# Kernel tuning notes

Measured on AMD Instinct MI355X. Metric: run time of the kernel, lower is better.

The kernel has to match this reference:

```python
import math
import jax, jax.numpy as jnp
import numpy as np

EPS_LN = 1e-5
EPS_NORM = 1e-12


def conv2d(x, w, b=None, groups=1):
    # x: (B,C,H,W), w: (O, I//groups, kh, kw)
    out = jax.lax.conv_general_dilated(
        x, w, window_strides=(1, 1), padding='SAME',
        dimension_numbers=('NCHW', 'OIHW', 'NCHW'),
        feature_group_count=groups)
    if b is not None:
        out = out + b[None, :, None, None]
    return out


def layernorm2d(x, w, b):
    # LayerNorm over channel dim of (B,C,H,W)
    mu = x.mean(axis=1, keepdims=True)
    var = ((x - mu) ** 2).mean(axis=1, keepdims=True)
    xn = (x - mu) / jnp.sqrt(var + EPS_LN)
    return xn * w[None, :, None, None] + b[None, :, None, None]


def l2norm(x):
    n = jnp.sqrt((x * x).sum(axis=-1, keepdims=True))
    return x / jnp.maximum(n, EPS_NORM)


def mha(s, Wi, bi, Wo, bo, num_heads):
    # torch nn.MultiheadAttention (batch_first) self-attention
    B, S, C = s.shape
    Dh = C // num_heads
    qkv = s @ Wi.T + bi                      # (B,S,3C)
    q, k, v = jnp.split(qkv, 3, axis=-1)
    hd = lambda t: t.reshape(B, S, num_heads, Dh).transpose(0, 2, 1, 3)
    q, k, v = hd(q), hd(k), hd(v)            # (B,H,S,Dh)
    attn = jax.nn.softmax(jnp.einsum('bhqd,bhkd->bhqk', q, k) / math.sqrt(Dh), axis=-1)
    o = jnp.einsum('bhqk,bhkd->bhqd', attn, v).transpose(0, 2, 1, 3).reshape(B, S, C)
    return o @ Wo.T + bo


def frfn(x, pconv_w, lin1_w, lin1_b, dw_w, dw_b, lin2_w, lin2_b):
    b, c, h, w = x.shape
    dc = c // 4
    x1 = conv2d(x[:, :dc], pconv_w)                       # partial conv, no bias
    x = jnp.concatenate([x1, x[:, dc:]], axis=1)
    xt = x.transpose(0, 2, 3, 1).reshape(b, h * w, c)
    y = jax.nn.gelu(xt @ lin1_w.T + lin1_b, approximate=False)  # (b,hw,2*hid)
    y1, y2 = jnp.split(y, 2, axis=-1)
    hid = lin1_w.shape[0] // 2
    y1 = y1.reshape(b, h, w, hid).transpose(0, 3, 1, 2)
    y1 = jax.nn.gelu(conv2d(y1, dw_w, dw_b, groups=hid), approximate=False)
    y1 = y1.transpose(0, 2, 3, 1).reshape(b, h * w, hid)
    out = (y1 * y2) @ lin2_w.T + lin2_b
    return out.reshape(b, h, w, c).transpose(0, 3, 1, 2)


def setup_inputs() -> dict:
    key = jax.random.key(0)
    ks = jax.random.split(key, 10)
    B, C, H, W = 16, 256, 64, 64
    HID = 2 * C  # FRFN hidden = embed_dim*2
    DC = C // 4
    w = lambda k, shape: (jax.random.normal(k, shape, dtype=jnp.float32) * 0.02)
    return {
        'x': jax.random.normal(ks[0], (B, C, H, W), dtype=jnp.float32),
        'slot_scale': jnp.asarray(C ** -0.5, dtype=jnp.float32),
        'norm1_w': jnp.ones((C,), jnp.float32), 'norm1_b': jnp.zeros((C,), jnp.float32),
        'in_proj_w': w(ks[1], (3 * C, C)), 'in_proj_b': jnp.zeros((3 * C,), jnp.float32),
        'out_proj_w': w(ks[2], (C, C)), 'out_proj_b': jnp.zeros((C,), jnp.float32),
        'norm2_w': jnp.ones((C,), jnp.float32), 'norm2_b': jnp.zeros((C,), jnp.float32),
        'pconv_w': w(ks[3], (DC, DC, 3, 3)),
        'lin1_w': w(ks[4], (2 * HID, C)), 'lin1_b': jnp.zeros((2 * HID,), jnp.float32),
        'dw_w': w(ks[5], (HID, 1, 3, 3)), 'dw_b': jnp.zeros((HID,), jnp.float32),
        'lin2_w': w(ks[6], (C, HID)), 'lin2_b': jnp.zeros((C,), jnp.float32),
    }


def reference(x, slot_scale, norm1_w, norm1_b, in_proj_w, in_proj_b,
              out_proj_w, out_proj_b, norm2_w, norm2_b,
              pconv_w, lin1_w, lin1_b, dw_w, dw_b, lin2_w, lin2_b):
    NUM_HEADS, POOL = 8, 8
    b, c, h, w = x.shape
    copy = x
    # ada_avgpool slot init: 8x8 exact block means (h,w divisible by pool)
    pooled = x.reshape(b, c, POOL, h // POOL, POOL, w // POOL).mean(axis=(3, 5))  # (b,c,8,8)
    init_slots = pooled.transpose(0, 2, 3, 1).reshape(b, POOL * POOL, c)          # (b,S,c)

    shortcut = x
    xn = layernorm2d(x, norm1_w, norm1_b)
    xf = xn.transpose(0, 2, 3, 1).reshape(b, h * w, c)                            # (b,N,c)
    logits = slot_scale * jnp.einsum('bsc,bnc->bsn', l2norm(init_slots), l2norm(xf))
    slots = jnp.einsum('bsn,bnc->bsc', jax.nn.softmax(logits, axis=-1), xf)
    slots = mha(slots, in_proj_w, in_proj_b, out_proj_w, out_proj_b, NUM_HEADS)
    out = jnp.einsum('bns,bsc->bnc', jax.nn.softmax(logits.transpose(0, 2, 1), axis=-1), slots)
    out = out.transpose(0, 2, 1).reshape(b, c, h, w)

    x = shortcut + out
    x = x + frfn(layernorm2d(x, norm2_w, norm2_b),
                 pconv_w, lin1_w, lin1_b, dw_w, dw_b, lin2_w, lin2_b)
    return (x, copy - x)
```

## Files before the change

### kernel.cpp

```cpp
#include <hip/hip_runtime.h>
#include <hip/hip_bf16.h>
#include <stdint.h>
#include <math.h>

#define BB 16
#define CC 256
#define HH 64
#define WW 64
#define NN 4096
#define SS 64
#define NHEAD 8
#define DH 32
#define HID 512
#define DC 64

typedef float    f32x4  __attribute__((ext_vector_type(4)));
typedef float    f32x2  __attribute__((ext_vector_type(2)));
typedef uint32_t u32x4  __attribute__((ext_vector_type(4)));
typedef uint16_t u16x8  __attribute__((ext_vector_type(8)));
typedef uint16_t u16x4  __attribute__((ext_vector_type(4)));
typedef uint16_t u16x2  __attribute__((ext_vector_type(2)));

__device__ __forceinline__ float gelu_fast(float x){
  float z = x * (1.5957691216057308f + 0.07135481627613705f * x * x);
  float e = __expf(z);
  float r = __builtin_amdgcn_rcpf(e + 1.0f);
  return x * e * r;
}
__device__ __forceinline__ uint16_t f2b(float f){
  union { float f; uint32_t u; } v; v.f = f;
  uint32_t r = v.u + 0x7fffu + ((v.u >> 16) & 1u);
  return (uint16_t)(r >> 16);
}
__device__ __forceinline__ float b2f(uint16_t h){
  union { uint32_t u; float f; } v; v.u = ((uint32_t)h) << 16;
  return v.f;
}
__device__ __forceinline__ f32x2 bpair(uint32_t u){
  union { uint32_t u; float f; } lo, hi;
  lo.u = u << 16; hi.u = u & 0xffff0000u;
  return (f32x2){lo.f, hi.f};
}

__device__ __forceinline__ float waveSum(float v){
#pragma unroll
  for (int m = 32; m >= 1; m >>= 1) v += __shfl_xor(v, m, 64);
  return v;
}
__device__ __forceinline__ float blockSum256(float v, float* s4){
  v = waveSum(v);
  __syncthreads();
  if ((threadIdx.x & 63) == 0) s4[threadIdx.x >> 6] = v;
  __syncthreads();
  return s4[0] + s4[1] + s4[2] + s4[3];
}

__device__ __forceinline__ void g2l16(const void* g, void* l){
  __builtin_amdgcn_global_load_lds((const __attribute__((address_space(1))) uint32_t*)g,
                                   (__attribute__((address_space(3))) uint32_t*)l, 16, 0, 0);
}

__device__ __forceinline__ int swz8(int row, int kp){ return (kp ^ (row & 7)) << 3; }

__device__ __forceinline__ void mfma_bf16(f32x4& d, u16x8 a, u16x8 b){
  asm volatile("v_mfma_f32_16x16x32_bf16 %0, %1, %2, %0" : "+v"(d) : "v"(a), "v"(b));
}

template<int SWA, int SWB>
__device__ __forceinline__ void mma_core(const uint16_t* lA, int lda, const uint16_t* lB, int ldb,
                                         f32x4 (&acc)[4][4], int wrow, int wcol, int lane){
  const int rb = lane & 15, ub = lane >> 4;
#pragma unroll
  for (int ks = 0; ks < 2; ks++){
    const int u = ks * 4 + ub;
    u16x8 af[4], bf[4];
#pragma unroll
    for (int m = 0; m < 4; m++){
      int r = wrow + m * 16 + rb;
      int e = SWA ? ((u ^ (r & 7)) << 3) : (u << 3);
      af[m] = *(const u16x8*)&lA[r * lda + e];
    }
#pragma unroll
    for (int n = 0; n < 4; n++){
      int r = wcol + n * 16 + rb;
      int e = SWB ? ((u ^ (r & 7)) << 3) : (u << 3);
      bf[n] = *(const u16x8*)&lB[r * ldb + e];
    }
#pragma unroll
    for (int m = 0; m < 4; m++)
#pragma unroll
      for (int n = 0; n < 4; n++)
        mfma_bf16(acc[m][n], af[m], bf[n]);
  }
}

__global__ __launch_bounds__(256) void k_t2b(const float* __restrict__ in, uint16_t* __restrict__ out){
  __shared__ float tile[64][33];
  int b = blockIdx.z;
  int n0 = blockIdx.x * 32;
  int c0 = blockIdx.y * 64;
  int tx = threadIdx.x, ty = threadIdx.y;
  const float* src = in + (size_t)b * CC * NN;
#pragma unroll
  for (int i = 0; i < 64; i += 8)
    tile[ty + i][tx] = src[(size_t)(c0 + ty + i) * NN + n0 + tx];
  __syncthreads();
  uint16_t* dst = out + (size_t)b * NN * CC;
#pragma unroll
  for (int i = 0; i < 32; i += 8){
    int r = ty + i;
    u16x2 o; o[0] = f2b(tile[tx * 2][r]); o[1] = f2b(tile[tx * 2 + 1][r]);
    *(u16x2*)&dst[(size_t)(n0 + r) * CC + c0 + tx * 2] = o;
  }
}

__global__ __launch_bounds__(256) void k_pool(const uint16_t* __restrict__ xhwcb, uint16_t* __restrict__ slotsNb){
  int bs = blockIdx.x; int b = bs >> 6, s = bs & 63;
  int sy = (s >> 3) * 8, sx = (s & 7) * 8;
  int t = threadIdx.x;
  int c4 = t & 63, pg = t >> 6;
  const uint16_t* base = xhwcb + (size_t)b * NN * CC;
  float a0 = 0.f, a1 = 0.f, a2 = 0.f, a3 = 0.f;
#pragma unroll
  for (int i = 0; i < 16; i++){
    int p = pg * 16 + i; int py = p >> 3, px = p & 7;
    u16x4 v = *(const u16x4*)&base[(size_t)((sy + py) * WW + sx + px) * CC + c4 * 4];
    a0 += b2f(v[0]); a1 += b2f(v[1]); a2 += b2f(v[2]); a3 += b2f(v[3]);
  }
  __shared__ float sm[4][64][4];
  sm[pg][c4][0] = a0; sm[pg][c4][1] = a1; sm[pg][c4][2] = a2; sm[pg][c4][3] = a3;
  __syncthreads();
  if (t < 64){
    float v0 = (sm[0][t][0] + sm[1][t][0] + sm[2][t][0] + sm[3][t][0]) * (1.0f / 64.0f);
    float v1 = (sm[0][t][1] + sm[1][t][1] + sm[2][t][1] + sm[3][t][1]) * (1.0f / 64.0f);
    float v2 = (sm[0][t][2] + sm[1][t][2] + sm[2][t][2] + sm[3][t][2]) * (1.0f / 64.0f);
    float v3 = (sm[0][t][3] + sm[1][t][3] + sm[2][t][3] + sm[3][t][3]) * (1.0f / 64.0f);
    float ss = waveSum(v0 * v0 + v1 * v1 + v2 * v2 + v3 * v3);
    float inv = 1.0f / fmaxf(sqrtf(ss), 1e-12f);
    u16x4 o; o[0] = f2b(v0 * inv); o[1] = f2b(v1 * inv); o[2] = f2b(v2 * inv); o[3] = f2b(v3 * inv);
    *(u16x4*)&slotsNb[(size_t)bs * CC + t * 4] = o;
  }
}

__global__ __launch_bounds__(256) void k_ln_w(const uint16_t* __restrict__ xa, const uint16_t* __restrict__ xb,
                                              const float* __restrict__ w, const float* __restrict__ b,
                                              uint16_t* __restrict__ xoutb, float* __restrict__ rn,
                                              uint16_t* __restrict__ xn2p){
  int row = blockIdx.x * 4 + (threadIdx.x >> 6);
  int lane = threadIdx.x & 63;
  u16x4 va = *(const u16x4*)&xa[(size_t)row * CC + lane * 4];
  float v0 = b2f(va[0]), v1 = b2f(va[1]), v2 = b2f(va[2]), v3 = b2f(va[3]);
  if (xb){
    u16x4 vb = *(const u16x4*)&xb[(size_t)row * CC + lane * 4];
    v0 += b2f(vb[0]); v1 += b2f(vb[1]); v2 += b2f(vb[2]); v3 += b2f(vb[3]);
  }
  float mu = waveSum(v0 + v1 + v2 + v3) * (1.0f / CC);
  float d0 = v0 - mu, d1 = v1 - mu, d2 = v2 - mu, d3 = v3 - mu;
  float var = waveSum(d0 * d0 + d1 * d1 + d2 * d2 + d3 * d3) * (1.0f / CC);
  float inv = rsqrtf(var + 1e-5f);
  float4 wv = *(const float4*)&w[lane * 4];
  float4 bv = *(const float4*)&b[lane * 4];
  float x0 = d0 * inv * wv.x + bv.x;
  float x1 = d1 * inv * wv.y + bv.y;
  float x2 = d2 * inv * wv.z + bv.z;
  float x3 = d3 * inv * wv.w + bv.w;
  u16x4 o; o[0] = f2b(x0); o[1] = f2b(x1); o[2] = f2b(x2); o[3] = f2b(x3);
  *(u16x4*)&xoutb[(size_t)row * CC + lane * 4] = o;
  if (xn2p && lane < 16){
    int bb = row >> 12, n = row & 4095, y = n >> 6, x = n & 63;
    *(u16x4*)&xn2p[(((size_t)(bb * 66 + y + 1)) * 66 + x + 1) * 64 + lane * 4] = o;
  }
  if (rn){
    float ss = waveSum(x0 * x0 + x1 * x1 + x2 * x2 + x3 * x3);
    if (lane == 0) rn[row] = 1.0f / fmaxf(sqrtf(ss), 1e-12f);
  }
}

__global__ __launch_bounds__(256) void k_zb(uint16_t* __restrict__ xn2p){
  int i = blockIdx.x * 256 + threadIdx.x;
  if (i >= 16 * 260 * 16) return;
  int c4 = i & 15; int rest = i >> 4;
  int j = rest % 260; int b = rest / 260;
  int py, px;
  if (j < 66){ py = 0; px = j; }
  else if (j < 132){ py = 65; px = j - 66; }
  else if (j < 196){ py = j - 132 + 1; px = 0; }
  else { py = j - 196 + 1; px = 65; }
  u16x4 z; z[0] = 0; z[1] = 0; z[2] = 0; z[3] = 0;
  *(u16x4*)&xn2p[(((size_t)(b * 66 + py)) * 66 + px) * 64 + c4 * 4] = z;
}

__global__ __launch_bounds__(256) void k_cvtw(const float* __restrict__ wi, const float* __restrict__ wo,
                                              const float* __restrict__ w1, const float* __restrict__ w2,
                                              const float* __restrict__ pw, const float* __restrict__ dww,
                                              uint16_t* __restrict__ wib, uint16_t* __restrict__ wob,
                                              uint16_t* __restrict__ w1b, uint16_t* __restrict__ w2b,
                                              uint16_t* __restrict__ wp2, float* __restrict__ dwwT){
  int i = blockIdx.x * 256 + threadIdx.x;
  if (i < 163840){
    const float* src; uint16_t* dst; int off;
    if (i < 49152){ src = wi; dst = wib; off = i; }
    else if (i < 65536){ src = wo; dst = wob; off = i - 49152; }
    else if (i < 131072){ src = w1; dst = w1b; off = i - 65536; }
    else { src = w2; dst = w2b; off = i - 131072; }
    float4 v = ((const float4*)src)[off];
    u16x4 o;
    o[0] = f2b(v.x); o[1] = f2b(v.y); o[2] = f2b(v.z); o[3] = f2b(v.w);
    *(u16x4*)&dst[(size_t)off * 4] = o;
  } else if (i < 200704){
    int j = i - 163840;
    if (j < 64 * 576){
      int co = j / 576, r = j % 576, tap = r >> 6, ci = r & 63;
      wp2[j] = f2b(pw[(size_t)co * 576 + ci * 9 + tap]);
    }
  } else {
    int j = i - 200704;
    if (j < 9 * HID){
      int tap = j / HID, ch = j % HID;
      dwwT[j] = dww[(size_t)ch * 9 + tap];
    }
  }
}

__global__ __launch_bounds__(256) void k_txT(const uint16_t* __restrict__ xnb, uint16_t* __restrict__ xnTb){
  __shared__ uint16_t tile[64 * 66];
  int b = blockIdx.z;
  int n0 = blockIdx.x * 64, c0 = blockIdx.y * 64;
  int t = threadIdx.x;
#pragma unroll
  for (int i = 0; i < 16; i++){
    int idx = i * 256 + t;
    int nr = idx >> 6, c = idx & 63;
    tile[c * 66 + nr] = xnb[((size_t)b * NN + n0 + nr) * CC + c0 + c];
  }
  __syncthreads();
#pragma unroll
  for (int i = 0; i < 16; i++){
    int idx = i * 256 + t;
    int cr = idx >> 6, n = idx & 63;
    xnTb[((size_t)b * CC + c0 + cr) * NN + n0 + n] = tile[cr * 66 + n];
  }
}

__global__ __launch_bounds__(256) void k_logits_mfma(const uint16_t* __restrict__ slotsNb,
                                                     const uint16_t* __restrict__ xnb,
                                                     const float* __restrict__ rn,
                                                     const float* __restrict__ scale_p,
                                                     uint16_t* __restrict__ E){
  __shared__ uint16_t smem[20480];
  __shared__ float rnS[256];
  uint16_t* lA = smem;
  uint16_t* lB = smem + 64 * 64;
  int t = threadIdx.x, lane = t & 63, w = t >> 6;
  int b = blockIdx.y, n0 = blockIdx.x * 256;
  rnS[t] = rn[b * NN + n0 + t];
  f32x4 acc[4][4];
#pragma unroll
  for (int m = 0; m < 4; m++)
#pragma unroll
    for (int n = 0; n < 4; n++) acc[m][n] = (f32x4){0.f, 0.f, 0.f, 0.f};
  for (int kc = 0; kc < 4; kc++){
#pragma unroll
    for (int i = 0; i < 2; i++){
      int idx = i * 256 + t, row = idx >> 3, kp = idx & 7;
      *(u16x8*)&lA[row * 64 + swz8(row, kp)] = *(const u16x8*)&slotsNb[(size_t)(b * 64 + row) * 256 + kc * 64 + kp * 8];
    }
#pragma unroll
    for (int i = 0; i < 8; i++){
      int idx = i * 256 + t, row = idx >> 3, kp = idx & 7;
      *(u16x8*)&lB[row * 64 + swz8(row, kp)] = *(const u16x8*)&xnb[((size_t)b * NN + n0 + row) * 256 + kc * 64 + kp * 8];
    }
    __syncthreads();
    mma_core<1, 1>(lA, 64, lB, 64, acc, 0, w * 64, lane);
    __syncthreads();
  }
  float scale = scale_p[0];
  int rb4 = (lane >> 4) * 4, cb = lane & 15;
#pragma unroll
  for (int m = 0; m < 4; m++)
#pragma unroll
    for (int n = 0; n < 4; n++)
#pragma unroll
      for (int j = 0; j < 4; j++){
        int s = m * 16 + rb4 + j, nl = w * 64 + n * 16 + cb;
        smem[s * 264 + nl] = f2b(__expf(acc[m][n][j] * scale * rnS[nl]));
      }
  __syncthreads();
#pragma unroll
  for (int i = 0; i < 8; i++){
    int idx = i * 256 + t, row = idx >> 5, cseg = idx & 31;
    *(u16x8*)&E[((size_t)b * 64 + row) * NN + n0 + cseg * 8] = *(const u16x8*)&smem[row * 264 + cseg * 8];
  }
}

__global__ __launch_bounds__(256) void k_z1(const uint16_t* __restrict__ E, float* __restrict__ invz1){
  int bs = blockIdx.x, t = threadIdx.x;
  u16x8 v0 = *(const u16x8*)&E[(size_t)bs * NN + t * 16];
  u16x8 v1 = *(const u16x8*)&E[(size_t)bs * NN + t * 16 + 8];
  float s = 0.f;
#pragma unroll
  for (int i = 0; i < 8; i++) s += b2f(v0[i]) + b2f(v1[i]);
  __shared__ float s4[4];
  float z = blockSum256(s, s4);
  if (t == 0) invz1[bs] = 1.0f / z;
}

__global__ __launch_bounds__(256) void k_slots_mfma(const uint16_t* __restrict__ E,
                                                    const uint16_t* __restrict__ xnTb,
                                                    float* __restrict__ part){
  __shared__ uint16_t lA[64 * 64];
  __shared__ uint16_t lB[256 * 64];
  int t = threadIdx.x, lane = t & 63, w = t >> 6;
  int ks = blockIdx.x, b = blockIdx.y;
  f32x4 acc[4][4];
#pragma unroll
  for (int m = 0; m < 4; m++)
#pragma unroll
    for (int n = 0; n < 4; n++) acc[m][n] = (f32x4){0.f, 0.f, 0.f, 0.f};
  for (int kc = 0; kc < 8; kc++){
    int n0 = ks * 512 + kc * 64;
#pragma unroll
    for (int i = 0; i < 2; i++){
      int q = (w * 2 + i) * 64 + lane;
      int row = q >> 3, kpe = swz8(row, q & 7);
      g2l16(&E[((size_t)b * 64 + row) * NN + n0 + kpe], &lA[(w * 2 + i) * 512]);
    }
#pragma unroll
    for (int i = 0; i < 8; i++){
      int q = (w * 8 + i) * 64 + lane;
      int row = q >> 3, kpe = swz8(row, q & 7);
      g2l16(&xnTb[((size_t)b * CC + row) * NN + n0 + kpe], &lB[(w * 8 + i) * 512]);
    }
    __syncthreads();
    mma_core<1, 1>(lA, 64, lB, 64, acc, 0, w * 64, lane);
    __syncthreads();
  }
  int rb4 = (lane >> 4) * 4, cb = lane & 15;
#pragma unroll
  for (int m = 0; m < 4; m++)
#pragma unroll
    for (int n = 0; n < 4; n++)
#pragma unroll
      for (int j = 0; j < 4; j++){
        int s = m * 16 + rb4 + j, c = w * 64 + n * 16 + cb;
        part[(((size_t)b * 8 + ks) * 64 + s) * 256 + c] = acc[m][n][j];
      }
}

__global__ __launch_bounds__(256) void k_fold(const float* __restrict__ part, const float* __restrict__ invz1,
                                              uint16_t* __restrict__ slotsb){
  int i = blockIdx.x * 256 + threadIdx.x;
  int row = i >> 6, c4 = i & 63;
  int b = row >> 6, s = row & 63;
  float4 a = {0.f, 0.f, 0.f, 0.f};
#pragma unroll
  for (int p = 0; p < 8; p++){
    float4 v = *(const float4*)&part[(((size_t)b * 8 + p) * 64 + s) * 256 + c4 * 4];
    a.x += v.x; a.y += v.y; a.z += v.z; a.w += v.w;
  }
  float iz = invz1[row];
  u16x4 o; o[0] = f2b(a.x * iz); o[1] = f2b(a.y * iz); o[2] = f2b(a.z * iz); o[3] = f2b(a.w * iz);
  *(u16x4*)&slotsb[(size_t)row * 256 + c4 * 4] = o;
}

__global__ __launch_bounds__(256) void k_gemm_qkv(const uint16_t* __restrict__ slotsb,
                                                  const uint16_t* __restrict__ wib,
                                                  const float* __restrict__ bi,
                                                  float* __restrict__ qkv){
  __shared__ uint16_t lA[128 * 64];
  __shared__ uint16_t lB[128 * 64];
  int t = threadIdx.x, lane = t & 63, w = t >> 6;
  int wrow = (w >> 1) * 64, wcol = (w & 1) * 64;
  int BR = blockIdx.x * 128, BC = blockIdx.y * 128;
  f32x4 acc[4][4];
#pragma unroll
  for (int m = 0; m < 4; m++)
#pragma unroll
    for (int n = 0; n < 4; n++) acc[m][n] = (f32x4){0.f, 0.f, 0.f, 0.f};
  for (int kc = 0; kc < 4; kc++){
#pragma unroll
    for (int i = 0; i < 4; i++){
      int idx = i * 256 + t, row = idx >> 3, kp = idx & 7;
      *(u16x8*)&lA[row * 64 + swz8(row, kp)] = *(const u16x8*)&slotsb[(size_t)(BR + row) * 256 + kc * 64 + kp * 8];
      *(u16x8*)&lB[row * 64 + swz8(row, kp)] = *(const u16x8*)&wib[(size_t)(BC + row) * 256 + kc * 64 + kp * 8];
    }
    __syncthreads();
    mma_core<1, 1>(lA, 64, lB, 64, acc, wrow, wcol, lane);
    __syncthreads();
  }
  int rb4 = (lane >> 4) * 4, cb = lane & 15;
#pragma unroll
  for (int m = 0; m < 4; m++)
#pragma unroll
    for (int n = 0; n < 4; n++){
      int c = BC + wcol + n * 16 + cb;
      float bias = bi[c];
#pragma unroll
      for (int j = 0; j < 4; j++)
        qkv[(size_t)(BR + wrow + m * 16 + rb4 + j) * 768 + c] = acc[m][n][j] + bias;
    }
}

__global__ __launch_bounds__(256) void k_attn(const float* __restrict__ qkv, uint16_t* __restrict__ aob){
  int b = blockIdx.x >> 3, h = blockIdx.x & 7;
  __shared__ float lq[64][33], lk[64][33], lv[64][33];
  __shared__ float sc[64][65];
  int t = threadIdx.x;
  for (int idx = t; idx < 64 * 32; idx += 256){
    int s = idx >> 5, d = idx & 31;
    const float* base = qkv + ((size_t)b * SS + s) * 768 + h * DH + d;
    lq[s][d] = base[0];
    lk[s][d] = base[256];
    lv[s][d] = base[512];
  }
  __syncthreads();
  const float rs = 0.17677669529663687f;
  for (int idx = t; idx < 64 * 64; idx += 256){
    int qq = idx >> 6, kk = idx & 63;
    float a = 0.f;
#pragma unroll
    for (int d = 0; d < 32; d++) a += lq[qq][d] * lk[kk][d];
    sc[qq][kk] = a * rs;
  }
  __syncthreads();
  {
    int r = t >> 2, sub = t & 3;
    float m = -1e30f;
#pragma unroll
    for (int k = sub * 16; k < sub * 16 + 16; k++) m = fmaxf(m, sc[r][k]);
    m = fmaxf(m, __shfl_xor(m, 1, 64));
    m = fmaxf(m, __shfl_xor(m, 2, 64));
    float z = 0.f;
#pragma unroll
    for (int k = sub * 16; k < sub * 16 + 16; k++){
      float e = __expf(sc[r][k] - m); sc[r][k] = e; z += e;
    }
    z += __shfl_xor(z, 1, 64);
    z += __shfl_xor(z, 2, 64);
    float iv = 1.0f / z;
#pragma unroll
    for (int k = sub * 16; k < sub * 16 + 16; k++) sc[r][k] *= iv;
  }
  __syncthreads();
  for (int idx = t; idx < 64 * 32; idx += 256){
    int qq = idx >> 5, d = idx & 31;
    float a = 0.f;
#pragma unroll
    for (int k = 0; k < 64; k++) a += sc[qq][k] * lv[k][d];
    aob[((size_t)b * SS + qq) * CC + h * DH + d] = f2b(a);
  }
}

__global__ __launch_bounds__(256) void k_gemm_oproj(const uint16_t* __restrict__ aob,
                                                    const uint16_t* __restrict__ wob,
                                                    const float* __restrict__ bo,
                                                    uint16_t* __restrict__ sl2Tb){
  __shared__ uint16_t lA[128 * 64];
  __shared__ uint16_t lB[128 * 64];
  int t = threadIdx.x, lane = t & 63, w = t >> 6;
  int wrow = (w >> 1) * 64, wcol = (w & 1) * 64;
  int BR = blockIdx.x * 128, BC = blockIdx.y * 128;
  f32x4 acc[4][4];
#pragma unroll
  for (int m = 0; m < 4; m++)
#pragma unroll
    for (int n = 0; n < 4; n++) acc[m][n] = (f32x4){0.f, 0.f, 0.f, 0.f};
  for (int kc = 0; kc < 4; kc++){
#pragma unroll
    for (int i = 0; i < 4; i++){
      int idx = i * 256 + t, row = idx >> 3, kp = idx & 7;
      *(u16x8*)&lA[row * 64 + swz8(row, kp)] = *(const u16x8*)&aob[(size_t)(BR + row) * 256 + kc * 64 + kp * 8];
      *(u16x8*)&lB[row * 64 + swz8(row, kp)] = *(const u16x8*)&wob[(size_t)(BC + row) * 256 + kc * 64 + kp * 8];
    }
    __syncthreads();
    mma_core<1, 1>(lA, 64, lB, 64, acc, wrow, wcol, lane);
    __syncthreads();
  }
  int rb4 = (lane >> 4) * 4, cb = lane & 15;
#pragma unroll
  for (int m = 0; m < 4; m++)
#pragma unroll
    for (int n = 0; n < 4; n++){
      int c = BC + wcol + n * 16 + cb;
      float bias = bo[c];
#pragma unroll
      for (int j = 0; j < 4; j++){
        int r = BR + wrow + m * 16 + rb4 + j;
        int b = r >> 6, s = r & 63;
        sl2Tb[((size_t)b * 256 + c) * 64 + s] = f2b(acc[m][n][j] + bias);
      }
    }
}

__global__ __launch_bounds__(256) void k_mix(const uint16_t* __restrict__ E, const uint16_t* __restrict__ sl2Tb,
                                             uint16_t* __restrict__ mixb){
  __shared__ uint16_t lA[128 * 72];
  __shared__ uint16_t lB[128 * 64];
  __shared__ float z2S[128];
  int t = threadIdx.x, lane = t & 63, w = t >> 6;
  int wrow = (w >> 1) * 64, wcol = (w & 1) * 64;
  int BR = blockIdx.x * 128, BC = blockIdx.y * 128, b = blockIdx.z;
#pragma unroll
  for (int i = 0; i < 4; i++){
    int idx = i * 256 + t; int s = idx >> 4, n8 = (idx & 15) * 8;
    u16x8 v = *(const u16x8*)&E[((size_t)b * 64 + s) * NN + BR + n8];
#pragma unroll
    for (int j = 0; j < 8; j++) lA[(n8 + j) * 72 + s] = v[j];
  }
#pragma unroll
  for (int i = 0; i < 4; i++){
    int idx = i * 256 + t, row = idx >> 3, kp = idx & 7;
    *(u16x8*)&lB[row * 64 + swz8(row, kp)] = *(const u16x8*)&sl2Tb[((size_t)b * 256 + BC + row) * 64 + kp * 8];
  }
  __syncthreads();
  if (t < 128){
    float s = 0.f;
#pragma unroll
    for (int k2 = 0; k2 < 64; k2++) s += b2f(lA[t * 72 + k2]);
    z2S[t] = 1.0f / s;
  }
  __syncthreads();
  f32x4 acc[4][4];
#pragma unroll
  for (int m = 0; m < 4; m++)
#pragma unroll
    for (int n = 0; n < 4; n++) acc[m][n] = (f32x4){0.f, 0.f, 0.f, 0.f};
  mma_core<0, 1>(lA, 72, lB, 64, acc, wrow, wcol, lane);
  int rb4 = (lane >> 4) * 4, cb = lane & 15;
#pragma unroll
  for (int m = 0; m < 4; m++)
#pragma unroll
    for (int n = 0; n < 4; n++)
#pragma unroll
      for (int j = 0; j < 4; j++){
        int lrow = wrow + m * 16 + rb4 + j;
        size_t gi = ((size_t)b * NN + BR + lrow) * 256 + BC + wcol + n * 16 + cb;
        mixb[gi] = f2b(acc[m][n][j] * z2S[lrow]);
      }
}

__global__ __launch_bounds__(256) void k_pconv_mfma(const uint16_t* __restrict__ xn2p,
                                                    const uint16_t* __restrict__ wp2,
                                                    uint16_t* __restrict__ pcb){
  __shared__ uint16_t lS[3328 * 8];
  __shared__ uint16_t lB[64 * 64];
  int t = threadIdx.x, lane = t & 63, w = t >> 6;
  int wrow = w * 64;
  int BR = blockIdx.x * 256;
  int b = BR >> 12, y0 = (BR & 4095) >> 6;
  size_t G0 = ((size_t)(b * 66 + y0) * 66) * 64;
#pragma unroll
  for (int i = 0; i < 13; i++){
    int q = i * 256 + t;
    int li = q >> 3, kp = q & 7;
    g2l16(&xn2p[G0 + (size_t)li * 64 + ((kp ^ (li & 7)) << 3)], &lS[q * 8]);
  }
  const int rb = lane & 15, ub = lane >> 4;
  int li0[4];
#pragma unroll
  for (int m = 0; m < 4; m++){
    int r = wrow + m * 16 + rb;
    li0[m] = ((r >> 6) + 1) * 66 + (r & 63) + 1;
  }
  f32x4 acc[4][4];
#pragma unroll
  for (int m = 0; m < 4; m++)
#pragma unroll
    for (int n = 0; n < 4; n++) acc[m][n] = (f32x4){0.f, 0.f, 0.f, 0.f};
#pragma unroll
  for (int tap = 0; tap < 9; tap++){
    const int doff = (tap / 3 - 1) * 66 + (tap % 3 - 1);
#pragma unroll
    for (int i = 0; i < 2; i++){
      int q = (w * 2 + i) * 64 + lane;
      int row = q >> 3, kpe = swz8(row, q & 7);
      g2l16(&wp2[(size_t)row * 576 + tap * 64 + kpe], &lB[(w * 2 + i) * 512]);
    }
    __syncthreads();
#pragma unroll
    for (int ks = 0; ks < 2; ks++){
      const int u = ks * 4 + ub;
      u16x8 af[4], bf[4];
#pragma unroll
      for (int m = 0; m < 4; m++){
        int li = li0[m] + doff;
        af[m] = *(const u16x8*)&lS[li * 64 + ((u ^ (li & 7)) << 3)];
      }
#pragma unroll
      for (int n = 0; n < 4; n++){
        int r = n * 16 + rb;
        bf[n] = *(const u16x8*)&lB[r * 64 + ((u ^ (r & 7)) << 3)];
      }
#pragma unroll
      for (int m = 0; m < 4; m++)
#pragma unroll
        for (int n = 0; n < 4; n++)
          mfma_bf16(acc[m][n], af[m], bf[n]);
    }
    __syncthreads();
  }
  int rb4 = (lane >> 4) * 4, cb = lane & 15;
#pragma unroll
  for (int m = 0; m < 4; m++)
#pragma unroll
    for (int j = 0; j < 4; j++){
      uint16_t* rp = &pcb[(size_t)(BR + wrow + m * 16 + rb4 + j) * 64 + cb];
#pragma unroll
      for (int n = 0; n < 4; n++)
        rp[n * 16] = f2b(acc[m][n][j]);
    }
}

__global__ __launch_bounds__(256) void k_lin1_mfma(const uint16_t* __restrict__ pcb,
                                                   const uint16_t* __restrict__ xn2b,
                                                   const uint16_t* __restrict__ w1b,
                                                   const float* __restrict__ b1,
                                                   uint16_t* __restrict__ Y1b, uint16_t* __restrict__ Y2b){
  __shared__ uint16_t lA[128 * 64];
  __shared__ uint16_t lB[128 * 64];
  int t = threadIdx.x, lane = t & 63, w = t >> 6;
  int wrow = (w >> 1) * 64, wcol = (w & 1) * 64;
  int bid = blockIdx.x;
  int xcd = bid & 7, i5 = bid >> 3;
  int BR = (xcd * 64 + (i5 >> 3)) * 128;
  int BC = (i5 & 7) * 128;
  f32x4 acc[4][4];
#pragma unroll
  for (int m = 0; m < 4; m++)
#pragma unroll
    for (int n = 0; n < 4; n++) acc[m][n] = (f32x4){0.f, 0.f, 0.f, 0.f};
  for (int kc = 0; kc < 4; kc++){
#pragma unroll
    for (int i = 0; i < 4; i++){
      int q = (w * 4 + i) * 64 + lane;
      int row = q >> 3, kpe = swz8(row, q & 7);
      size_t gr = (size_t)(BR + row);
      const uint16_t* src = (kc == 0) ? &pcb[gr * 64 + kpe] : &xn2b[gr * 256 + kc * 64 + kpe];
      g2l16(src, &lA[(w * 4 + i) * 512]);
      g2l16(&w1b[(size_t)(BC + row) * 256 + kc * 64 + kpe], &lB[(w * 4 + i) * 512]);
    }
    __syncthreads();
    mma_core<1, 1>(lA, 64, lB, 64, acc, wrow, wcol, lane);
    __syncthreads();
  }
  int rb4 = (lane >> 4) * 4, cb = lane & 15;
  float bias[4];
#pragma unroll
  for (int n = 0; n < 4; n++) bias[n] = b1[BC + wcol + n * 16 + cb];
  uint16_t* dst = (BC < HID) ? (Y1b + BC + wcol + cb) : (Y2b + (BC - HID) + wcol + cb);
#pragma unroll
  for (int m = 0; m < 4; m++)
#pragma unroll
    for (int j = 0; j < 4; j++){
      uint16_t* rp = dst + (size_t)(BR + wrow + m * 16 + rb4 + j) * HID;
#pragma unroll
      for (int n = 0; n < 4; n++)
        rp[n * 16] = f2b(gelu_fast(acc[m][n][j] + bias[n]));
    }
}

__global__ __launch_bounds__(256) void k_dwconv(const uint16_t* __restrict__ Y1b,
                                                const float* __restrict__ dwwT,
                                                const float* __restrict__ dwb,
                                                const uint16_t* __restrict__ Y2b,
                                                uint16_t* __restrict__ YPb){
  __shared__ uint16_t lds[3 * 18 * 136];
  int b = blockIdx.z, chunk = blockIdx.y;
  int y = blockIdx.x >> 2, seg = blockIdx.x & 3;
  int x0 = seg * 16;
  int t = threadIdx.x;
  const uint16_t* base = Y1b + (size_t)b * NN * HID + chunk * 128;
  const u16x8 z = {0, 0, 0, 0, 0, 0, 0, 0};
#pragma unroll
  for (int i = 0; i < 4; i++){
    int idx = i * 256 + t;
    if (idx < 864){
      int g8 = idx & 15, rest = idx >> 4;
      int c = rest % 18, r = rest / 18;
      int ry = y + r - 1, xx = x0 + c - 1;
      u16x8 v = z;
      if (ry >= 0 && ry < HH && xx >= 0 && xx < WW)
        v = *(const u16x8*)&base[(size_t)(ry * WW + xx) * HID + g8 * 8];
      *(u16x8*)&lds[(r * 18 + c) * 136 + g8 * 8] = v;
    }
  }
  __syncthreads();
  int px = t >> 4, g8 = t & 15;
  int cg = chunk * 128 + g8 * 8;
  int n = y * WW + x0 + px;
  u32x4 y2v = *(const u32x4*)&Y2b[((size_t)b * NN + n) * HID + cg];
  f32x2 acc2[4];
  {
    float4 b0 = *(const float4*)&dwb[cg];
    float4 b1 = *(const float4*)&dwb[cg + 4];
    acc2[0] = (f32x2){b0.x, b0.y}; acc2[1] = (f32x2){b0.z, b0.w};
    acc2[2] = (f32x2){b1.x, b1.y}; acc2[3] = (f32x2){b1.z, b1.w};
  }
#pragma unroll
  for (int r = 0; r < 3; r++)
#pragma unroll
    for (int dx = 0; dx < 3; dx++){
      u32x4 v = *(const u32x4*)&lds[(r * 18 + px + dx) * 136 + g8 * 8];
      const f32x2* wt = (const f32x2*)&dwwT[(r * 3 + dx) * HID + cg];
      acc2[0] += bpair(v[0]) * wt[0];
      acc2[1] += bpair(v[1]) * wt[1];
      acc2[2] += bpair(v[2]) * wt[2];
      acc2[3] += bpair(v[3]) * wt[3];
    }
  u16x8 o;
#pragma unroll
  for (int j = 0; j < 4; j++){
    f32x2 yy = bpair(y2v[j]);
    float g0 = gelu_fast(acc2[j].x) * yy.x;
    float g1 = gelu_fast(acc2[j].y) * yy.y;
    o[2 * j] = f2b(g0); o[2 * j + 1] = f2b(g1);
  }
  *(u16x8*)&YPb[((size_t)b * NN + n) * HID + cg] = o;
}

__global__ __launch_bounds__(256) void k_lin2_mfma(const uint16_t* __restrict__ YPb,
                                                   const uint16_t* __restrict__ w2b,
                                                   const float* __restrict__ b2,
                                                   uint16_t* __restrict__ deltab){
  __shared__ uint16_t lA[128 * 64];
  __shared__ uint16_t lB[128 * 64];
  int t = threadIdx.x, lane = t & 63, w = t >> 6;
  int wrow = (w >> 1) * 64, wcol = (w & 1) * 64;
  int bid = blockIdx.x;
  int xcd = bid & 7, i5 = bid >> 3;
  int BR = (xcd * 64 + (i5 >> 1)) * 128;
  int BC = (i5 & 1) * 128;
  f32x4 acc[4][4];
#pragma unroll
  for (int m = 0; m < 4; m++)
#pragma unroll
    for (int n = 0; n < 4; n++) acc[m][n] = (f32x4){0.f, 0.f, 0.f, 0.f};
  for (int kc = 0; kc < 8; kc++){
#pragma unroll
    for (int i = 0; i < 4; i++){
      int q = (w * 4 + i) * 64 + lane;
      int row = q >> 3, kpe = swz8(row, q & 7);
      g2l16(&YPb[(size_t)(BR + row) * HID + kc * 64 + kpe], &lA[(w * 4 + i) * 512]);
      g2l16(&w2b[(size_t)(BC + row) * HID + kc * 64 + kpe], &lB[(w * 4 + i) * 512]);
    }
    __syncthreads();
    mma_core<1, 1>(lA, 64, lB, 64, acc, wrow, wcol, lane);
    __syncthreads();
  }
  int rb4 = (lane >> 4) * 4, cb = lane & 15;
  float bias[4];
#pragma unroll
  for (int n = 0; n < 4; n++) bias[n] = b2[BC + wcol + n * 16 + cb];
  uint16_t* dst = deltab + BC + wcol + cb;
#pragma unroll
  for (int m = 0; m < 4; m++)
#pragma unroll
    for (int j = 0; j < 4; j++){
      uint16_t* rp = dst + (size_t)(BR + wrow + m * 16 + rb4 + j) * CC;
#pragma unroll
      for (int n = 0; n < 4; n++)
        rp[n * 16] = f2b(acc[m][n][j] + bias[n]);
    }
}

__global__ __launch_bounds__(256) void k_final2(const uint16_t* __restrict__ mixb,
                                                const uint16_t* __restrict__ deltab,
                                                const uint16_t* __restrict__ xhwcb,
                                                float* __restrict__ out){
  __shared__ float t0[64 * 68];
  __shared__ float t1[64 * 68];
  int b = blockIdx.z;
  int n0 = blockIdx.x * 64, c0 = blockIdx.y * 64;
  int t = threadIdx.x;
#pragma unroll
  for (int i = 0; i < 4; i++){
    int idx = i * 256 + t, row = idx >> 4, c4 = idx & 15;
    size_t gp = ((size_t)b * NN + n0 + row) * CC + c0 + c4 * 4;
    u16x4 m = *(const u16x4*)&mixb[gp];
    u16x4 d = *(const u16x4*)&deltab[gp];
    u16x4 xh = *(const u16x4*)&xhwcb[gp];
    f32x4 v0, v1;
#pragma unroll
    for (int j = 0; j < 4; j++){
      float v = b2f(m[j]) + b2f(d[j]);
      v0[j] = b2f(xh[j]) + v;
      v1[j] = -v;
    }
    *(f32x4*)&t0[row * 68 + c4 * 4] = v0;
    *(f32x4*)&t1[row * 68 + c4 * 4] = v1;
  }
  __syncthreads();
  int cl = t >> 2, seg = t & 3;
  float* o1 = out + (size_t)BB * CC * NN;
  size_t gbase = ((size_t)(b * CC + c0 + cl)) * NN + n0 + seg * 16;
#pragma unroll
  for (int k = 0; k < 4; k++){
    float4 a, c;
    a.x = t0[(seg * 16 + k * 4 + 0) * 68 + cl];
    a.y = t0[(seg * 16 + k * 4 + 1) * 68 + cl];
    a.z = t0[(seg * 16 + k * 4 + 2) * 68 + cl];
    a.w = t0[(seg * 16 + k * 4 + 3) * 68 + cl];
    c.x = t1[(seg * 16 + k * 4 + 0) * 68 + cl];
    c.y = t1[(seg * 16 + k * 4 + 1) * 68 + cl];
    c.z = t1[(seg * 16 + k * 4 + 2) * 68 + cl];
    c.w = t1[(seg * 16 + k * 4 + 3) * 68 + cl];
    *(float4*)&out[gbase + k * 4] = a;
    *(float4*)&o1[gbase + k * 4] = c;
  }
}

extern "C" void kernel_launch(void* const* d_in, const int* in_sizes, int n_in,
                              void* d_out, int out_size, void* d_ws, size_t ws_size,
                              hipStream_t stream){
  const float* x       = (const float*)d_in[0];
  const float* scale_p = (const float*)d_in[1];
  const float* n1w     = (const float*)d_in[2];
  const float* n1b     = (const float*)d_in[3];
  const float* wi      = (const float*)d_in[4];
  const float* bi      = (const float*)d_in[5];
  const float* wo      = (const float*)d_in[6];
  const float* bo      = (const float*)d_in[7];
  const float* n2w     = (const float*)d_in[8];
  const float* n2b     = (const float*)d_in[9];
  const float* pw      = (const float*)d_in[10];
  const float* w1      = (const float*)d_in[11];
  const float* b1      = (const float*)d_in[12];
  const float* dww     = (const float*)d_in[13];
  const float* dwb     = (const float*)d_in[14];
  const float* w2      = (const float*)d_in[15];
  const float* b2      = (const float*)d_in[16];

  float* base = (float*)d_ws;
  size_t off = 0;
  float* part = base + off; off += (size_t)BB * 8 * SS * CC;
  float* QKV  = base + off; off += (size_t)BB * SS * 3 * CC;
  float* RN   = base + off; off += (size_t)BB * NN;
  float* IZ1  = base + off; off += (size_t)BB * SS;
  float* dwwT = base + off; off += (size_t)9 * HID;
  uint16_t* slotsNb = (uint16_t*)(base + off); off += (size_t)BB * SS * CC / 2;
  uint16_t* slotsb  = (uint16_t*)(base + off); off += (size_t)BB * SS * CC / 2;
  uint16_t* aob     = (uint16_t*)(base + off); off += (size_t)BB * SS * CC / 2;
  uint16_t* sl2Tb   = (uint16_t*)(base + off); off += (size_t)BB * CC * SS / 2;
  uint16_t* xhwcb   = (uint16_t*)(base + off); off += (size_t)BB * NN * CC / 2;
  uint16_t* xnb     = (uint16_t*)(base + off); off += (size_t)BB * NN * CC / 2;
  uint16_t* xnTb    = (uint16_t*)(base + off); off += (size_t)BB * NN * CC / 2;
  uint16_t* mixb    = (uint16_t*)(base + off); off += (size_t)BB * NN * CC / 2;
  uint16_t* deltab  = (uint16_t*)(base + off); off += (size_t)BB * NN * CC / 2;
  uint16_t* E       = (uint16_t*)(base + off); off += (size_t)BB * SS * NN / 2;
  uint16_t* w1b     = (uint16_t*)(base + off); off += (size_t)(2 * HID) * CC / 2;
  uint16_t* w2b     = (uint16_t*)(base + off); off += (size_t)CC * HID / 2;
  uint16_t* wib     = (uint16_t*)(base + off); off += (size_t)(3 * CC) * CC / 2;
  uint16_t* wob     = (uint16_t*)(base + off); off += (size_t)CC * CC / 2;
  uint16_t* wp2     = (uint16_t*)(base + off); off += (size_t)64 * 576 / 2 + 16;
  uint16_t* Y1b     = (uint16_t*)(base + off); off += (size_t)BB * NN * HID / 2;
  uint16_t* Y2b     = (uint16_t*)(base + off); off += (size_t)BB * NN * HID / 2;
  uint16_t* YPb     = (uint16_t*)(base + off); off += (size_t)BB * NN * HID / 2;
  uint16_t* xn2b    = (uint16_t*)(base + off); off += (size_t)BB * NN * CC / 2;
  uint16_t* xn2p    = (uint16_t*)(base + off); off += (size_t)BB * 66 * 66 * 64 / 2;
  uint16_t* pcb     = (uint16_t*)(base + off); off += (size_t)BB * NN * 64 / 2;
  if (ws_size < off * sizeof(float)) return;
  float* OUT = (float*)d_out;

  dim3 tb2(32, 8);
  k_t2b<<<dim3(NN / 32, CC / 64, BB), tb2, 0, stream>>>(x, xhwcb);
  k_pool<<<BB * SS, 256, 0, stream>>>(xhwcb, slotsNb);
  k_ln_w<<<BB * NN / 4, 256, 0, stream>>>(xhwcb, (const uint16_t*)nullptr, n1w, n1b, xnb, RN,
                                          (uint16_t*)nullptr);
  k_cvtw<<<803, 256, 0, stream>>>(wi, wo, w1, w2, pw, dww, wib, wob, w1b, w2b, wp2, dwwT);
  k_zb<<<(16 * 260 * 16 + 255) / 256, 256, 0, stream>>>(xn2p);
  k_logits_mfma<<<dim3(NN / 256, BB), 256, 0, stream>>>(slotsNb, xnb, RN, scale_p, E);
  k_txT<<<dim3(NN / 64, CC / 64, BB), 256, 0, stream>>>(xnb, xnTb);
  k_z1<<<BB * SS, 256, 0, stream>>>(E, IZ1);
  k_slots_mfma<<<dim3(8, BB), 256, 0, stream>>>(E, xnTb, part);
  k_fold<<<(BB * SS * CC / 4) / 256, 256, 0, stream>>>(part, IZ1, slotsb);
  k_gemm_qkv<<<dim3(8, 6), 256, 0, stream>>>(slotsb, wib, bi, QKV);
  k_attn<<<BB * NHEAD, 256, 0, stream>>>(QKV, aob);
  k_gemm_oproj<<<dim3(8, 2), 256, 0, stream>>>(aob, wob, bo, sl2Tb);
  k_mix<<<dim3(NN / 128, CC / 128, BB), 256, 0, stream>>>(E, sl2Tb, mixb);
  k_ln_w<<<BB * NN / 4, 256, 0, stream>>>(xhwcb, mixb, n2w, n2b, xn2b, (float*)nullptr, xn2p);
  k_pconv_mfma<<<BB * NN / 256, 256, 0, stream>>>(xn2p, wp2, pcb);
  k_lin1_mfma<<<4096, 256, 0, stream>>>(pcb, xn2b, w1b, b1, Y1b, Y2b);
  k_dwconv<<<dim3(256, 4, BB), 256, 0, stream>>>(Y1b, dwwT, dwb, Y2b, YPb);
  k_lin2_mfma<<<1024, 256, 0, stream>>>(YPb, w2b, b2, deltab);
  k_final2<<<dim3(NN / 64, CC / 64, BB), 256, 0, stream>>>(mixb, deltab, xhwcb, OUT);
}
```

Measured before the change: 409.1 us.

## Compute two pixels per thread in depthwise conv with packed FMA

The depthwise 3x3 conv kernel now handles a 32-pixel strip per block instead of 16, and each thread computes two adjacent pixels. Each thread loads four LDS columns per row and reuses the two overlapping ones, and each weight load now serves two pixels. Accumulation uses inline v_pk_fma_f32. The aim is to cut halo loads, LDS reads and weight loads per output, at the cost of more registers, a larger LDS tile and half as many blocks.

```diff
diff --git a/kernel.cpp b/kernel.cpp
--- a/kernel.cpp
+++ b/kernel.cpp
@@ -40,6 +40,9 @@
   union { uint32_t u; float f; } lo, hi;
   lo.u = u << 16; hi.u = u & 0xffff0000u;
   return (f32x2){lo.f, hi.f};
+}
+__device__ __forceinline__ void pkfma(f32x2& d, f32x2 a, f32x2 b){
+  asm("v_pk_fma_f32 %0, %1, %2, %0" : "+v"(d) : "v"(a), "v"(b));
 }
 
 __device__ __forceinline__ float waveSum(float v){
@@ -664,58 +667,73 @@
                                                 const float* __restrict__ dwb,
                                                 const uint16_t* __restrict__ Y2b,
                                                 uint16_t* __restrict__ YPb){
-  __shared__ uint16_t lds[3 * 18 * 136];
+  __shared__ uint16_t lds[3 * 34 * 136];
   int b = blockIdx.z, chunk = blockIdx.y;
-  int y = blockIdx.x >> 2, seg = blockIdx.x & 3;
-  int x0 = seg * 16;
+  int y = blockIdx.x >> 1, seg = blockIdx.x & 1;
+  int x0 = seg * 32;
   int t = threadIdx.x;
   const uint16_t* base = Y1b + (size_t)b * NN * HID + chunk * 128;
-  const u16x8 z = {0, 0, 0, 0, 0, 0, 0, 0};
-#pragma unroll
-  for (int i = 0; i < 4; i++){
+  const u16x8 z8 = {0, 0, 0, 0, 0, 0, 0, 0};
+#pragma unroll
+  for (int i = 0; i < 7; i++){
     int idx = i * 256 + t;
-    if (idx < 864){
+    if (idx < 1632){
       int g8 = idx & 15, rest = idx >> 4;
-      int c = rest % 18, r = rest / 18;
+      int c = rest % 34, r = rest / 34;
       int ry = y + r - 1, xx = x0 + c - 1;
-      u16x8 v = z;
+      u16x8 v = z8;
       if (ry >= 0 && ry < HH && xx >= 0 && xx < WW)
         v = *(const u16x8*)&base[(size_t)(ry * WW + xx) * HID + g8 * 8];
-      *(u16x8*)&lds[(r * 18 + c) * 136 + g8 * 8] = v;
-    }
-  }
-  __syncthreads();
-  int px = t >> 4, g8 = t & 15;
+      *(u16x8*)&lds[(r * 34 + c) * 136 + g8 * 8] = v;
+    }
+  }
+  __syncthreads();
+  int pg = t >> 4, g8 = t & 15;
   int cg = chunk * 128 + g8 * 8;
-  int n = y * WW + x0 + px;
-  u32x4 y2v = *(const u32x4*)&Y2b[((size_t)b * NN + n) * HID + cg];
-  f32x2 acc2[4];
+  int px = pg * 2;
+  f32x2 acc[2][4];
   {
     float4 b0 = *(const float4*)&dwb[cg];
     float4 b1 = *(const float4*)&dwb[cg + 4];
-    acc2[0] = (f32x2){b0.x, b0.y}; acc2[1] = (f32x2){b0.z, b0.w};
-    acc2[2] = (f32x2){b1.x, b1.y}; acc2[3] = (f32x2){b1.z, b1.w};
-  }
-#pragma unroll
-  for (int r = 0; r < 3; r++)
+    acc[0][0] = (f32x2){b0.x, b0.y}; acc[0][1] = (f32x2){b0.z, b0.w};
+    acc[0][2] = (f32x2){b1.x, b1.y}; acc[0][3] = (f32x2){b1.z, b1.w};
+#pragma unroll
+    for (int j = 0; j < 4; j++) acc[1][j] = acc[0][j];
+  }
+#pragma unroll
+  for (int r = 0; r < 3; r++){
+    f32x2 u[4][4];
+#pragma unroll
+    for (int cc = 0; cc < 4; cc++){
+      u32x4 v = *(const u32x4*)&lds[(r * 34 + px + cc) * 136 + g8 * 8];
+#pragma unroll
+      for (int j = 0; j < 4; j++) u[cc][j] = bpair(v[j]);
+    }
 #pragma unroll
     for (int dx = 0; dx < 3; dx++){
-      u32x4 v = *(const u32x4*)&lds[(r * 18 + px + dx) * 136 + g8 * 8];
       const f32x2* wt = (const f32x2*)&dwwT[(r * 3 + dx) * HID + cg];
-      acc2[0] += bpair(v[0]) * wt[0];
-      acc2[1] += bpair(v[1]) * wt[1];
-      acc2[2] += bpair(v[2]) * wt[2];
-      acc2[3] += bpair(v[3]) * wt[3];
-    }
-  u16x8 o;
-#pragma unroll
-  for (int j = 0; j < 4; j++){
-    f32x2 yy = bpair(y2v[j]);
-    float g0 = gelu_fast(acc2[j].x) * yy.x;
-    float g1 = gelu_fast(acc2[j].y) * yy.y;
-    o[2 * j] = f2b(g0); o[2 * j + 1] = f2b(g1);
-  }
-  *(u16x8*)&YPb[((size_t)b * NN + n) * HID + cg] = o;
+      f32x2 w0 = wt[0], w1 = wt[1], w2 = wt[2], w3 = wt[3];
+      pkfma(acc[0][0], u[dx][0], w0);     pkfma(acc[1][0], u[dx + 1][0], w0);
+      pkfma(acc[0][1], u[dx][1], w1);     pkfma(acc[1][1], u[dx + 1][1], w1);
+      pkfma(acc[0][2], u[dx][2], w2);     pkfma(acc[1][2], u[dx + 1][2], w2);
+      pkfma(acc[0][3], u[dx][3], w3);     pkfma(acc[1][3], u[dx + 1][3], w3);
+    }
+  }
+  int n = y * WW + x0 + px;
+  const uint16_t* y2p = &Y2b[((size_t)b * NN + n) * HID + cg];
+  uint16_t* yp = &YPb[((size_t)b * NN + n) * HID + cg];
+#pragma unroll
+  for (int p = 0; p < 2; p++){
+    u32x4 y2v = *(const u32x4*)(y2p + (size_t)p * HID);
+    u16x8 o;
+#pragma unroll
+    for (int j = 0; j < 4; j++){
+      f32x2 yy = bpair(y2v[j]);
+      o[2 * j]     = f2b(gelu_fast(acc[p][j].x) * yy.x);
+      o[2 * j + 1] = f2b(gelu_fast(acc[p][j].y) * yy.y);
+    }
+    *(u16x8*)(yp + (size_t)p * HID) = o;
+  }
 }
 
 __global__ __launch_bounds__(256) void k_lin2_mfma(const uint16_t* __restrict__ YPb,
@@ -880,7 +898,7 @@
   k_ln_w<<<BB * NN / 4, 256, 0, stream>>>(xhwcb, mixb, n2w, n2b, xn2b, (float*)nullptr, xn2p);
   k_pconv_mfma<<<BB * NN / 256, 256, 0, stream>>>(xn2p, wp2, pcb);
   k_lin1_mfma<<<4096, 256, 0, stream>>>(pcb, xn2b, w1b, b1, Y1b, Y2b);
-  k_dwconv<<<dim3(256, 4, BB), 256, 0, stream>>>(Y1b, dwwT, dwb, Y2b, YPb);
+  k_dwconv<<<dim3(128, 4, BB), 256, 0, stream>>>(Y1b, dwwT, dwb, Y2b, YPb);
   k_lin2_mfma<<<1024, 256, 0, stream>>>(YPb, w2b, b2, deltab);
   k_final2<<<dim3(NN / 64, CC / 64, BB), 256, 0, stream>>>(mixb, deltab, xhwcb, OUT);
 }
```

Result: no change. 407.5 us (-0.4%).
